# Optimization experiments

Measured on AMD Instinct MI355X. Metric: run time of the kernel, lower is better.

Reference implementation:

```python
import jax, jax.numpy as jnp
import numpy as np

N_NODES = 50000
N_EDGES = 800000
HID = 64
F_NODE = 64
F_EDGE = 16
DEC_H = 64
EPS = 1e-5


def setup_inputs() -> dict:
    key = jax.random.key(0)
    ks = jax.random.split(key, 16)
    inp = {}
    inp['x'] = jax.random.normal(ks[0], (N_NODES, F_NODE), dtype=jnp.float32)
    inp['edge_index'] = jax.random.randint(ks[1], (2, N_EDGES), 0, N_NODES, dtype=jnp.int32)
    inp['edge_attr'] = jax.random.normal(ks[2], (N_EDGES, F_EDGE), dtype=jnp.float32)
    # 3 GCN layers (F_NODE == HID so weights stack)
    inp['conv_w'] = jax.random.normal(ks[3], (3, HID, HID), dtype=jnp.float32) / np.sqrt(HID)
    inp['conv_b'] = jnp.zeros((3, HID), dtype=jnp.float32)
    inp['ln_g'] = jnp.ones((3, HID), dtype=jnp.float32)
    inp['ln_b'] = jnp.zeros((3, HID), dtype=jnp.float32)
    dec_in = 2 * HID + F_EDGE
    inp['dec_w1'] = jax.random.normal(ks[4], (dec_in, DEC_H), dtype=jnp.float32) / np.sqrt(dec_in)
    inp['dec_b1'] = jnp.zeros((DEC_H,), dtype=jnp.float32)
    inp['dec_w2'] = jax.random.normal(ks[5], (DEC_H, DEC_H // 2), dtype=jnp.float32) / np.sqrt(DEC_H)
    inp['dec_b2'] = jnp.zeros((DEC_H // 2,), dtype=jnp.float32)
    inp['dec_w3'] = jax.random.normal(ks[6], (DEC_H // 2, 1), dtype=jnp.float32) / np.sqrt(DEC_H // 2)
    inp['dec_b3'] = jnp.zeros((1,), dtype=jnp.float32)
    return inp


def _layer_norm(h, g, b):
    mu = jnp.mean(h, axis=-1, keepdims=True)
    var = jnp.mean(jnp.square(h - mu), axis=-1, keepdims=True)
    return (h - mu) * jax.lax.rsqrt(var + EPS) * g + b


def _forward(x, edge_index, edge_attr, conv_w, conv_b, ln_g, ln_b,
             dec_w1, dec_b1, dec_w2, dec_b2, dec_w3, dec_b3):
    n = x.shape[0]
    src, dst = edge_index[0], edge_index[1]
    # add self-loops (PyG GCNConv default)
    loop = jnp.arange(n, dtype=edge_index.dtype)
    src_sl = jnp.concatenate([src, loop])
    dst_sl = jnp.concatenate([dst, loop])
    # symmetric normalization: deg over target column (incl. self-loops)
    deg = jax.ops.segment_sum(jnp.ones_like(src_sl, dtype=x.dtype), dst_sl, num_segments=n)
    dinv = jnp.where(deg > 0, jax.lax.rsqrt(deg), 0.0)
    norm = dinv[src_sl] * dinv[dst_sl]  # (E+N,)

    h = x
    for l in range(conv_w.shape[0]):
        t = h @ conv_w[l]                                   # (N, H)
        msg = t[src_sl] * norm[:, None]                     # (E+N, H)
        agg = jax.ops.segment_sum(msg, dst_sl, num_segments=n) + conv_b[l]
        h = jax.nn.relu(_layer_norm(agg, ln_g[l], ln_b[l]))
        # dropout is identity at inference

    # edge decoder: concat(src_emb, dst_emb, edge_attr) -> MLP -> scalar
    z = jnp.concatenate([h[src], h[dst], edge_attr], axis=-1)  # (E, 2H+Fe)
    z = jax.nn.relu(z @ dec_w1 + dec_b1)
    z = jax.nn.relu(z @ dec_w2 + dec_b2)
    return (z @ dec_w3 + dec_b3).squeeze(-1)                   # (E,)


def reference(x, edge_index, edge_attr, conv_w, conv_b, ln_g, ln_b,
              dec_w1, dec_b1, dec_w2, dec_b2, dec_w3, dec_b3):
    return _forward(x, edge_index, edge_attr, conv_w, conv_b, ln_g, ln_b,
                    dec_w1, dec_b1, dec_w2, dec_b2, dec_w3, dec_b3)
```

## Files before the change

### kernel.cpp

```cpp
#include <hip/hip_runtime.h>
#include <hip/hip_fp16.h>

#define N_NODES 50000
#define N_EDGES 800000
#define HID 64
#define F_EDGE 16
#define LN_EPS 1e-5f
#define SCAN_BLOCKS ((N_NODES + 255) / 256)

__device__ inline float wave_sum64(float v) {
    #pragma unroll
    for (int o = 32; o > 0; o >>= 1) v += __shfl_xor(v, o, 64);
    return v;
}

__global__ void k_zero_cnt(int* __restrict__ cnt) {
    int i = blockIdx.x * blockDim.x + threadIdx.x;
    if (i < N_NODES) cnt[i] = 0;
}

__global__ void k_count(const int* __restrict__ dst, int* __restrict__ cnt) {
    int e = blockIdx.x * blockDim.x + threadIdx.x;
    if (e < N_EDGES) atomicAdd(&cnt[dst[e]], 1);
}

__global__ void k_scan1(const int* __restrict__ cnt, int* __restrict__ row_ptr,
                        int* __restrict__ bsum, float* __restrict__ dinv) {
    __shared__ int wsum[4];
    int tid = threadIdx.x, lane = tid & 63, w = tid >> 6;
    int i = blockIdx.x * 256 + tid;
    int v = (i < N_NODES) ? cnt[i] : 0;
    if (i < N_NODES) dinv[i] = rsqrtf((float)v + 1.0f);
    int isc = v;
    #pragma unroll
    for (int o = 1; o < 64; o <<= 1) {
        int n = __shfl_up(isc, o, 64);
        if (lane >= o) isc += n;
    }
    if (lane == 63) wsum[w] = isc;
    __syncthreads();
    int woff = 0;
    #pragma unroll
    for (int k = 0; k < 4; k++) woff += (k < w) ? wsum[k] : 0;
    if (i < N_NODES) row_ptr[i] = woff + isc - v;
    if (tid == 255) bsum[blockIdx.x] = woff + isc;
}

__global__ void k_scan2(const int* __restrict__ bsum, int* __restrict__ boff) {
    __shared__ int wsum[4];
    int tid = threadIdx.x, lane = tid & 63, w = tid >> 6;
    int v = (tid < SCAN_BLOCKS) ? bsum[tid] : 0;
    int isc = v;
    #pragma unroll
    for (int o = 1; o < 64; o <<= 1) {
        int n = __shfl_up(isc, o, 64);
        if (lane >= o) isc += n;
    }
    if (lane == 63) wsum[w] = isc;
    __syncthreads();
    int woff = 0;
    #pragma unroll
    for (int k = 0; k < 4; k++) woff += (k < w) ? wsum[k] : 0;
    if (tid < SCAN_BLOCKS) boff[tid] = woff + isc - v;
}

__global__ void k_scan3(int* __restrict__ row_ptr, const int* __restrict__ boff,
                        int* __restrict__ cursor) {
    int i = blockIdx.x * blockDim.x + threadIdx.x;
    if (i < N_NODES) {
        int r = row_ptr[i] + boff[i >> 8];
        row_ptr[i] = r;
        cursor[i] = r;
    }
    if (i == 0) row_ptr[N_NODES] = N_EDGES;
}

__global__ void k_fill(const int* __restrict__ src, const int* __restrict__ dst,
                       const float* __restrict__ dinv, int* __restrict__ cursor,
                       int* __restrict__ col, float* __restrict__ ew) {
    int e = blockIdx.x * blockDim.x + threadIdx.x;
    if (e < N_EDGES) {
        int s = src[e], d = dst[e];
        int pos = atomicAdd(&cursor[d], 1);
        col[pos] = s;
        ew[pos] = dinv[s] * dinv[d];
    }
}

__global__ void __launch_bounds__(256)
k_gemm_reg(const float* __restrict__ hin, const float* __restrict__ W,
           __half* __restrict__ out) {
    int lane = threadIdx.x & 63;
    int wid = (blockIdx.x * blockDim.x + threadIdx.x) >> 6;
    int nwaves = (gridDim.x * blockDim.x) >> 6;
    float w[64];
    #pragma unroll
    for (int k = 0; k < 64; k++) w[k] = W[k * 64 + lane];
    for (int row = wid; row < N_NODES; row += nwaves) {
        int r = __builtin_amdgcn_readfirstlane(row);
        const float* xr = hin + r * 64;
        float acc = 0.0f;
        #pragma unroll
        for (int k = 0; k < 64; k++) acc = fmaf(xr[k], w[k], acc);
        out[r * 64 + lane] = __float2half_rn(acc);
    }
}

__global__ void __launch_bounds__(256)
k_gemm_pq(const float* __restrict__ hin, const float* __restrict__ Wp,
          const float* __restrict__ bp, const float* __restrict__ Wq,
          __half* __restrict__ P, __half* __restrict__ Q) {
    int half_g = gridDim.x >> 1;
    bool isQ = (blockIdx.x >= half_g);
    const float* W = isQ ? Wq : Wp;
    __half* out = isQ ? Q : P;
    int lane = threadIdx.x & 63;
    int bid = isQ ? (blockIdx.x - half_g) : blockIdx.x;
    int wid = (bid * blockDim.x + threadIdx.x) >> 6;
    int nwaves = (half_g * blockDim.x) >> 6;
    float w[64];
    #pragma unroll
    for (int k = 0; k < 64; k++) w[k] = W[k * 64 + lane];
    float binit = isQ ? 0.0f : bp[lane];
    for (int row = wid; row < N_NODES; row += nwaves) {
        int r = __builtin_amdgcn_readfirstlane(row);
        const float* xr = hin + r * 64;
        float acc = binit;
        #pragma unroll
        for (int k = 0; k < 64; k++) acc = fmaf(xr[k], w[k], acc);
        out[r * 64 + lane] = __float2half_rn(acc);
    }
}

__global__ void __launch_bounds__(256)
k_gather_ln(const __half* __restrict__ t, const float* __restrict__ dinv,
            const int* __restrict__ row_ptr, const int* __restrict__ col,
            const float* __restrict__ ew, const float* __restrict__ cb,
            const float* __restrict__ g, const float* __restrict__ b,
            float* __restrict__ h) {
    int gid = blockIdx.x * blockDim.x + threadIdx.x;
    int node = gid >> 6, lane = gid & 63;
    if (node >= N_NODES) return;
    int n0 = __builtin_amdgcn_readfirstlane(node);
    int q = lane >> 3;
    int c8 = lane & 7;
    const float4* t4 = (const float4*)t;

    float acc[8];
    #pragma unroll
    for (int u = 0; u < 8; u++) acc[u] = 0.0f;

    if (q == 0) {
        float di = dinv[n0];
        float s2 = di * di;
        float4 raw = t4[(size_t)n0 * 8 + c8];
        const __half2* hp = (const __half2*)&raw;
        const float4* cb4 = (const float4*)cb;
        float4 cb0 = cb4[2 * c8], cb1 = cb4[2 * c8 + 1];
        float2 f0 = __half22float2(hp[0]);
        float2 f1 = __half22float2(hp[1]);
        float2 f2 = __half22float2(hp[2]);
        float2 f3 = __half22float2(hp[3]);
        acc[0] = fmaf(f0.x, s2, cb0.x); acc[1] = fmaf(f0.y, s2, cb0.y);
        acc[2] = fmaf(f1.x, s2, cb0.z); acc[3] = fmaf(f1.y, s2, cb0.w);
        acc[4] = fmaf(f2.x, s2, cb1.x); acc[5] = fmaf(f2.y, s2, cb1.y);
        acc[6] = fmaf(f3.x, s2, cb1.z); acc[7] = fmaf(f3.y, s2, cb1.w);
    }

    int beg = row_ptr[n0], end = row_ptr[n0 + 1];
    int deg = end - beg;

    int cL = 0; float wL = 0.0f;
    if (lane < deg) { cL = col[beg + lane]; wL = ew[beg + lane]; }
    int steps = (min(deg, 64) + 7) >> 3;

    #pragma unroll 4
    for (int st = 0; st < steps; st++) {
        int idx = 8 * st + q;
        int s = __shfl(cL, idx, 64);
        float wgt = __shfl(wL, idx, 64);
        float4 raw = t4[(size_t)s * 8 + c8];
        const __half2* hp = (const __half2*)&raw;
        float2 f0 = __half22float2(hp[0]);
        float2 f1 = __half22float2(hp[1]);
        float2 f2 = __half22float2(hp[2]);
        float2 f3 = __half22float2(hp[3]);
        acc[0] = fmaf(f0.x, wgt, acc[0]); acc[1] = fmaf(f0.y, wgt, acc[1]);
        acc[2] = fmaf(f1.x, wgt, acc[2]); acc[3] = fmaf(f1.y, wgt, acc[3]);
        acc[4] = fmaf(f2.x, wgt, acc[4]); acc[5] = fmaf(f2.y, wgt, acc[5]);
        acc[6] = fmaf(f3.x, wgt, acc[6]); acc[7] = fmaf(f3.y, wgt, acc[7]);
    }
    for (int j = beg + 64 + q; j < end; j += 8) {
        int s = col[j];
        float wgt = ew[j];
        float4 raw = t4[(size_t)s * 8 + c8];
        const __half2* hp = (const __half2*)&raw;
        float2 f0 = __half22float2(hp[0]);
        float2 f1 = __half22float2(hp[1]);
        float2 f2 = __half22float2(hp[2]);
        float2 f3 = __half22float2(hp[3]);
        acc[0] = fmaf(f0.x, wgt, acc[0]); acc[1] = fmaf(f0.y, wgt, acc[1]);
        acc[2] = fmaf(f1.x, wgt, acc[2]); acc[3] = fmaf(f1.y, wgt, acc[3]);
        acc[4] = fmaf(f2.x, wgt, acc[4]); acc[5] = fmaf(f2.y, wgt, acc[5]);
        acc[6] = fmaf(f3.x, wgt, acc[6]); acc[7] = fmaf(f3.y, wgt, acc[7]);
    }

    #pragma unroll
    for (int o = 8; o <= 32; o <<= 1) {
        #pragma unroll
        for (int u = 0; u < 8; u++) acc[u] += __shfl_xor(acc[u], o, 64);
    }

    float ps = 0.0f;
    #pragma unroll
    for (int u = 0; u < 8; u++) ps += acc[u];
    float mu = wave_sum64(ps) * (1.0f / 512.0f);
    float dd[8], vps = 0.0f;
    #pragma unroll
    for (int u = 0; u < 8; u++) { dd[u] = acc[u] - mu; vps += dd[u] * dd[u]; }
    float var = wave_sum64(vps) * (1.0f / 512.0f);
    float rstd = rsqrtf(var + LN_EPS);

    if (q == 0) {
        const float4* g4 = (const float4*)g;
        const float4* b4 = (const float4*)b;
        float4 g0 = g4[2 * c8], g1 = g4[2 * c8 + 1];
        float4 b0 = b4[2 * c8], b1v = b4[2 * c8 + 1];
        float4 y0, y1;
        y0.x = fmaxf(fmaf(dd[0] * rstd, g0.x, b0.x), 0.f);
        y0.y = fmaxf(fmaf(dd[1] * rstd, g0.y, b0.y), 0.f);
        y0.z = fmaxf(fmaf(dd[2] * rstd, g0.z, b0.z), 0.f);
        y0.w = fmaxf(fmaf(dd[3] * rstd, g0.w, b0.w), 0.f);
        y1.x = fmaxf(fmaf(dd[4] * rstd, g1.x, b1v.x), 0.f);
        y1.y = fmaxf(fmaf(dd[5] * rstd, g1.y, b1v.y), 0.f);
        y1.z = fmaxf(fmaf(dd[6] * rstd, g1.z, b1v.z), 0.f);
        y1.w = fmaxf(fmaf(dd[7] * rstd, g1.w, b1v.w), 0.f);
        float4* h4 = (float4*)h;
        h4[(size_t)n0 * 16 + 2 * c8] = y0;
        h4[(size_t)n0 * 16 + 2 * c8 + 1] = y1;
    }
}

__global__ void __launch_bounds__(256)
k_decoder(const __half* __restrict__ P, const __half* __restrict__ Q,
          const int* __restrict__ src, const int* __restrict__ dst,
          const float* __restrict__ attr,
          const float* __restrict__ W1c,
          const float* __restrict__ W2, const float* __restrict__ b2,
          const float* __restrict__ W3, const float* __restrict__ b3,
          float* __restrict__ out) {
    int e = blockIdx.x * blockDim.x + threadIdx.x;
    if (e >= N_EDGES) return;
    int s = src[e], d = dst[e];

    const float4* ap = (const float4*)(attr + (size_t)e * 16);
    float4 av0 = ap[0], av1 = ap[1], av2 = ap[2], av3 = ap[3];

    float acc[64];
    const float4* Pp = (const float4*)(P + (size_t)s * 64);
    const float4* Qp = (const float4*)(Q + (size_t)d * 64);
    #pragma unroll
    for (int c = 0; c < 8; c++) {
        float4 pv = Pp[c], qv = Qp[c];
        const __half2* ph = (const __half2*)&pv;
        const __half2* qh = (const __half2*)&qv;
        #pragma unroll
        for (int u = 0; u < 4; u++) {
            float2 pf = __half22float2(ph[u]);
            float2 qf = __half22float2(qh[u]);
            acc[8 * c + 2 * u]     = pf.x + qf.x;
            acc[8 * c + 2 * u + 1] = pf.y + qf.y;
        }
    }

    #pragma unroll
    for (int j = 0; j < 64; j++) {
        float a = acc[j];
        a = fmaf(av0.x, W1c[0 * 64 + j], a);
        a = fmaf(av0.y, W1c[1 * 64 + j], a);
        a = fmaf(av0.z, W1c[2 * 64 + j], a);
        a = fmaf(av0.w, W1c[3 * 64 + j], a);
        a = fmaf(av1.x, W1c[4 * 64 + j], a);
        a = fmaf(av1.y, W1c[5 * 64 + j], a);
        a = fmaf(av1.z, W1c[6 * 64 + j], a);
        a = fmaf(av1.w, W1c[7 * 64 + j], a);
        a = fmaf(av2.x, W1c[8 * 64 + j], a);
        a = fmaf(av2.y, W1c[9 * 64 + j], a);
        a = fmaf(av2.z, W1c[10 * 64 + j], a);
        a = fmaf(av2.w, W1c[11 * 64 + j], a);
        a = fmaf(av3.x, W1c[12 * 64 + j], a);
        a = fmaf(av3.y, W1c[13 * 64 + j], a);
        a = fmaf(av3.z, W1c[14 * 64 + j], a);
        a = fmaf(av3.w, W1c[15 * 64 + j], a);
        acc[j] = fmaxf(a, 0.0f);
    }

    float acc2[32];
    #pragma unroll
    for (int j = 0; j < 32; j++) acc2[j] = b2[j];
    #pragma unroll
    for (int k = 0; k < 64; k++) {
        float hk = acc[k];
        #pragma unroll
        for (int j = 0; j < 32; j++)
            acc2[j] = fmaf(hk, W2[k * 32 + j], acc2[j]);
    }

    float o = b3[0];
    #pragma unroll
    for (int j = 0; j < 32; j++)
        o = fmaf(fmaxf(acc2[j], 0.0f), W3[j], o);
    out[e] = o;
}

extern "C" void kernel_launch(void* const* d_in, const int* in_sizes, int n_in,
                              void* d_out, int out_size, void* d_ws, size_t ws_size,
                              hipStream_t stream) {
    const float* x      = (const float*)d_in[0];
    const int*   ei     = (const int*)d_in[1];
    const float* attr   = (const float*)d_in[2];
    const float* conv_w = (const float*)d_in[3];
    const float* conv_b = (const float*)d_in[4];
    const float* ln_g   = (const float*)d_in[5];
    const float* ln_b   = (const float*)d_in[6];
    const float* dw1    = (const float*)d_in[7];
    const float* db1    = (const float*)d_in[8];
    const float* dw2    = (const float*)d_in[9];
    const float* db2    = (const float*)d_in[10];
    const float* dw3    = (const float*)d_in[11];
    const float* db3    = (const float*)d_in[12];
    float* out = (float*)d_out;

    const int* src = ei;
    const int* dst = ei + N_EDGES;

    char* p = (char*)d_ws;
    float*  dinv    = (float*)p;  p += sizeof(float) * N_NODES;
    float*  h       = (float*)p;  p += sizeof(float) * (size_t)N_NODES * 64;
    __half* t_h     = (__half*)p; p += sizeof(__half) * (size_t)N_NODES * 64;
    __half* P_h     = (__half*)p; p += sizeof(__half) * (size_t)N_NODES * 64;
    __half* Q_h     = (__half*)p; p += sizeof(__half) * (size_t)N_NODES * 64;
    int*    cnt     = (int*)p;    p += sizeof(int) * N_NODES;
    int*    cursor  = (int*)p;    p += sizeof(int) * N_NODES;
    int*    row_ptr = (int*)p;    p += sizeof(int) * (N_NODES + 1);
    int*    col     = (int*)p;    p += sizeof(int) * N_EDGES;
    float*  ew      = (float*)p;  p += sizeof(float) * N_EDGES;
    int*    bsum    = (int*)p;    p += sizeof(int) * 256;
    int*    boff    = (int*)p;    p += sizeof(int) * 256;

    const int nb_nodes = (N_NODES + 255) / 256;
    const int nb_edges = (N_EDGES + 255) / 256;

    k_zero_cnt<<<nb_nodes, 256, 0, stream>>>(cnt);
    k_count<<<nb_edges, 256, 0, stream>>>(dst, cnt);
    k_scan1<<<SCAN_BLOCKS, 256, 0, stream>>>(cnt, row_ptr, bsum, dinv);
    k_scan2<<<1, 256, 0, stream>>>(bsum, boff);
    k_scan3<<<nb_nodes, 256, 0, stream>>>(row_ptr, boff, cursor);
    k_fill<<<nb_edges, 256, 0, stream>>>(src, dst, dinv, cursor, col, ew);

    const int gemm_blocks = 1024;
    const int gather_blocks = N_NODES / 4;

    const float* hin = x;
    for (int l = 0; l < 3; l++) {
        k_gemm_reg<<<gemm_blocks, 256, 0, stream>>>(hin, conv_w + l * 4096, t_h);
        k_gather_ln<<<gather_blocks, 256, 0, stream>>>(
            t_h, dinv, row_ptr, col, ew, conv_b + l * 64,
            ln_g + l * 64, ln_b + l * 64, h);
        hin = h;
    }

    k_gemm_pq<<<2 * gemm_blocks, 256, 0, stream>>>(h, dw1, db1, dw1 + 64 * 64, P_h, Q_h);

    k_decoder<<<nb_edges, 256, 0, stream>>>(
        P_h, Q_h, src, dst, attr, dw1 + 128 * 64, dw2, db2, dw3, db3, out);
}
```

Measured before the change: 476.9 us.

## Reorder GCN layer to aggregate pre-scaled features before GEMM and fuse LayerNorm

Each GCN layer now runs aggregate-then-transform. Node features are pre-scaled by dinv and stored as fp16, so the gather sums neighbours without per-edge weights, and the edge-weight array and its loads go away. LayerNorm, ReLU and bias move into the GEMM kernel, which writes the next layer's dinv-scaled fp16 features directly. The cost is an extra element-wise init kernel, an fp32 agg buffer written and read between the two kernels each layer, and fp16 storage of the pre-scaled inputs, which may change precision slightly.

```diff
diff --git a/kernel.cpp b/kernel.cpp
--- a/kernel.cpp
+++ b/kernel.cpp
@@ -76,33 +76,127 @@
 }
 
 __global__ void k_fill(const int* __restrict__ src, const int* __restrict__ dst,
-                       const float* __restrict__ dinv, int* __restrict__ cursor,
-                       int* __restrict__ col, float* __restrict__ ew) {
+                       int* __restrict__ cursor, int* __restrict__ col) {
     int e = blockIdx.x * blockDim.x + threadIdx.x;
     if (e < N_EDGES) {
         int s = src[e], d = dst[e];
         int pos = atomicAdd(&cursor[d], 1);
         col[pos] = s;
-        ew[pos] = dinv[s] * dinv[d];
-    }
+    }
+}
+
+__global__ void k_xs_init(const float* __restrict__ x, const float* __restrict__ dinv,
+                          __half* __restrict__ xs) {
+    int i = blockIdx.x * blockDim.x + threadIdx.x;
+    if (i < N_NODES * 64) xs[i] = __float2half_rn(x[i] * dinv[i >> 6]);
 }
 
 __global__ void __launch_bounds__(256)
-k_gemm_reg(const float* __restrict__ hin, const float* __restrict__ W,
-           __half* __restrict__ out) {
+k_gather_agg(const __half* __restrict__ xs, const float* __restrict__ dinv,
+             const int* __restrict__ row_ptr, const int* __restrict__ col,
+             float* __restrict__ agg) {
+    int gid = blockIdx.x * blockDim.x + threadIdx.x;
+    int node = gid >> 6, lane = gid & 63;
+    if (node >= N_NODES) return;
+    int n0 = __builtin_amdgcn_readfirstlane(node);
+    int q = lane >> 3;
+    int c8 = lane & 7;
+    const float4* x4 = (const float4*)xs;
+
+    float acc[8];
+    #pragma unroll
+    for (int u = 0; u < 8; u++) acc[u] = 0.0f;
+
+    if (q == 0) {
+        float4 raw = x4[(size_t)n0 * 8 + c8];
+        const __half2* hp = (const __half2*)&raw;
+        float2 f0 = __half22float2(hp[0]);
+        float2 f1 = __half22float2(hp[1]);
+        float2 f2 = __half22float2(hp[2]);
+        float2 f3 = __half22float2(hp[3]);
+        acc[0] = f0.x; acc[1] = f0.y; acc[2] = f1.x; acc[3] = f1.y;
+        acc[4] = f2.x; acc[5] = f2.y; acc[6] = f3.x; acc[7] = f3.y;
+    }
+
+    int beg = row_ptr[n0], end = row_ptr[n0 + 1];
+    int deg = end - beg;
+
+    int cL = 0;
+    if (lane < deg) cL = col[beg + lane];
+    int steps = (min(deg, 64) + 7) >> 3;
+
+    #pragma unroll 4
+    for (int st = 0; st < steps; st++) {
+        int idx = 8 * st + q;
+        int s = __shfl(cL, idx, 64);
+        float m = (idx < deg) ? 1.0f : 0.0f;
+        float4 raw = x4[(size_t)s * 8 + c8];
+        const __half2* hp = (const __half2*)&raw;
+        float2 f0 = __half22float2(hp[0]);
+        float2 f1 = __half22float2(hp[1]);
+        float2 f2 = __half22float2(hp[2]);
+        float2 f3 = __half22float2(hp[3]);
+        acc[0] = fmaf(f0.x, m, acc[0]); acc[1] = fmaf(f0.y, m, acc[1]);
+        acc[2] = fmaf(f1.x, m, acc[2]); acc[3] = fmaf(f1.y, m, acc[3]);
+        acc[4] = fmaf(f2.x, m, acc[4]); acc[5] = fmaf(f2.y, m, acc[5]);
+        acc[6] = fmaf(f3.x, m, acc[6]); acc[7] = fmaf(f3.y, m, acc[7]);
+    }
+    for (int j = beg + 64 + q; j < end; j += 8) {
+        int s = col[j];
+        float4 raw = x4[(size_t)s * 8 + c8];
+        const __half2* hp = (const __half2*)&raw;
+        float2 f0 = __half22float2(hp[0]);
+        float2 f1 = __half22float2(hp[1]);
+        float2 f2 = __half22float2(hp[2]);
+        float2 f3 = __half22float2(hp[3]);
+        acc[0] += f0.x; acc[1] += f0.y; acc[2] += f1.x; acc[3] += f1.y;
+        acc[4] += f2.x; acc[5] += f2.y; acc[6] += f3.x; acc[7] += f3.y;
+    }
+
+    #pragma unroll
+    for (int o = 8; o <= 32; o <<= 1) {
+        #pragma unroll
+        for (int u = 0; u < 8; u++) acc[u] += __shfl_xor(acc[u], o, 64);
+    }
+
+    if (q == 0) {
+        float di = dinv[n0];
+        float4 y0, y1;
+        y0.x = acc[0] * di; y0.y = acc[1] * di; y0.z = acc[2] * di; y0.w = acc[3] * di;
+        y1.x = acc[4] * di; y1.y = acc[5] * di; y1.z = acc[6] * di; y1.w = acc[7] * di;
+        float4* a4 = (float4*)agg;
+        a4[(size_t)n0 * 16 + 2 * c8] = y0;
+        a4[(size_t)n0 * 16 + 2 * c8 + 1] = y1;
+    }
+}
+
+__global__ void __launch_bounds__(256)
+k_gemm_ln(const float* __restrict__ agg, const float* __restrict__ W,
+          const float* __restrict__ cb, const float* __restrict__ g,
+          const float* __restrict__ b, const float* __restrict__ dinv,
+          __half* __restrict__ xs_out, float* __restrict__ h_out) {
     int lane = threadIdx.x & 63;
     int wid = (blockIdx.x * blockDim.x + threadIdx.x) >> 6;
     int nwaves = (gridDim.x * blockDim.x) >> 6;
     float w[64];
     #pragma unroll
     for (int k = 0; k < 64; k++) w[k] = W[k * 64 + lane];
+    float cbl = cb[lane], gl = g[lane], bl = b[lane];
     for (int row = wid; row < N_NODES; row += nwaves) {
         int r = __builtin_amdgcn_readfirstlane(row);
-        const float* xr = hin + r * 64;
-        float acc = 0.0f;
+        const float* xr = agg + r * 64;
+        float acc = cbl;
         #pragma unroll
         for (int k = 0; k < 64; k++) acc = fmaf(xr[k], w[k], acc);
-        out[r * 64 + lane] = __float2half_rn(acc);
+        float mu = wave_sum64(acc) * (1.0f / 64.0f);
+        float d = acc - mu;
+        float var = wave_sum64(d * d) * (1.0f / 64.0f);
+        float y = fmaxf(fmaf(d * rsqrtf(var + LN_EPS), gl, bl), 0.0f);
+        if (xs_out) {
+            xs_out[r * 64 + lane] = __float2half_rn(y * dinv[r]);
+        } else {
+            h_out[r * 64 + lane] = y;
+        }
     }
 }
 
@@ -129,115 +223,6 @@
         #pragma unroll
         for (int k = 0; k < 64; k++) acc = fmaf(xr[k], w[k], acc);
         out[r * 64 + lane] = __float2half_rn(acc);
-    }
-}
-
-__global__ void __launch_bounds__(256)
-k_gather_ln(const __half* __restrict__ t, const float* __restrict__ dinv,
-            const int* __restrict__ row_ptr, const int* __restrict__ col,
-            const float* __restrict__ ew, const float* __restrict__ cb,
-            const float* __restrict__ g, const float* __restrict__ b,
-            float* __restrict__ h) {
-    int gid = blockIdx.x * blockDim.x + threadIdx.x;
-    int node = gid >> 6, lane = gid & 63;
-    if (node >= N_NODES) return;
-    int n0 = __builtin_amdgcn_readfirstlane(node);
-    int q = lane >> 3;
-    int c8 = lane & 7;
-    const float4* t4 = (const float4*)t;
-
-    float acc[8];
-    #pragma unroll
-    for (int u = 0; u < 8; u++) acc[u] = 0.0f;
-
-    if (q == 0) {
-        float di = dinv[n0];
-        float s2 = di * di;
-        float4 raw = t4[(size_t)n0 * 8 + c8];
-        const __half2* hp = (const __half2*)&raw;
-        const float4* cb4 = (const float4*)cb;
-        float4 cb0 = cb4[2 * c8], cb1 = cb4[2 * c8 + 1];
-        float2 f0 = __half22float2(hp[0]);
-        float2 f1 = __half22float2(hp[1]);
-        float2 f2 = __half22float2(hp[2]);
-        float2 f3 = __half22float2(hp[3]);
-        acc[0] = fmaf(f0.x, s2, cb0.x); acc[1] = fmaf(f0.y, s2, cb0.y);
-        acc[2] = fmaf(f1.x, s2, cb0.z); acc[3] = fmaf(f1.y, s2, cb0.w);
-        acc[4] = fmaf(f2.x, s2, cb1.x); acc[5] = fmaf(f2.y, s2, cb1.y);
-        acc[6] = fmaf(f3.x, s2, cb1.z); acc[7] = fmaf(f3.y, s2, cb1.w);
-    }
-
-    int beg = row_ptr[n0], end = row_ptr[n0 + 1];
-    int deg = end - beg;
-
-    int cL = 0; float wL = 0.0f;
-    if (lane < deg) { cL = col[beg + lane]; wL = ew[beg + lane]; }
-    int steps = (min(deg, 64) + 7) >> 3;
-
-    #pragma unroll 4
-    for (int st = 0; st < steps; st++) {
-        int idx = 8 * st + q;
-        int s = __shfl(cL, idx, 64);
-        float wgt = __shfl(wL, idx, 64);
-        float4 raw = t4[(size_t)s * 8 + c8];
-        const __half2* hp = (const __half2*)&raw;
-        float2 f0 = __half22float2(hp[0]);
-        float2 f1 = __half22float2(hp[1]);
-        float2 f2 = __half22float2(hp[2]);
-        float2 f3 = __half22float2(hp[3]);
-        acc[0] = fmaf(f0.x, wgt, acc[0]); acc[1] = fmaf(f0.y, wgt, acc[1]);
-        acc[2] = fmaf(f1.x, wgt, acc[2]); acc[3] = fmaf(f1.y, wgt, acc[3]);
-        acc[4] = fmaf(f2.x, wgt, acc[4]); acc[5] = fmaf(f2.y, wgt, acc[5]);
-        acc[6] = fmaf(f3.x, wgt, acc[6]); acc[7] = fmaf(f3.y, wgt, acc[7]);
-    }
-    for (int j = beg + 64 + q; j < end; j += 8) {
-        int s = col[j];
-        float wgt = ew[j];
-        float4 raw = t4[(size_t)s * 8 + c8];
-        const __half2* hp = (const __half2*)&raw;
-        float2 f0 = __half22float2(hp[0]);
-        float2 f1 = __half22float2(hp[1]);
-        float2 f2 = __half22float2(hp[2]);
-        float2 f3 = __half22float2(hp[3]);
-        acc[0] = fmaf(f0.x, wgt, acc[0]); acc[1] = fmaf(f0.y, wgt, acc[1]);
-        acc[2] = fmaf(f1.x, wgt, acc[2]); acc[3] = fmaf(f1.y, wgt, acc[3]);
-        acc[4] = fmaf(f2.x, wgt, acc[4]); acc[5] = fmaf(f2.y, wgt, acc[5]);
-        acc[6] = fmaf(f3.x, wgt, acc[6]); acc[7] = fmaf(f3.y, wgt, acc[7]);
-    }
-
-    #pragma unroll
-    for (int o = 8; o <= 32; o <<= 1) {
-        #pragma unroll
-        for (int u = 0; u < 8; u++) acc[u] += __shfl_xor(acc[u], o, 64);
-    }
-
-    float ps = 0.0f;
-    #pragma unroll
-    for (int u = 0; u < 8; u++) ps += acc[u];
-    float mu = wave_sum64(ps) * (1.0f / 512.0f);
-    float dd[8], vps = 0.0f;
-    #pragma unroll
-    for (int u = 0; u < 8; u++) { dd[u] = acc[u] - mu; vps += dd[u] * dd[u]; }
-    float var = wave_sum64(vps) * (1.0f / 512.0f);
-    float rstd = rsqrtf(var + LN_EPS);
-
-    if (q == 0) {
-        const float4* g4 = (const float4*)g;
-        const float4* b4 = (const float4*)b;
-        float4 g0 = g4[2 * c8], g1 = g4[2 * c8 + 1];
-        float4 b0 = b4[2 * c8], b1v = b4[2 * c8 + 1];
-        float4 y0, y1;
-        y0.x = fmaxf(fmaf(dd[0] * rstd, g0.x, b0.x), 0.f);
-        y0.y = fmaxf(fmaf(dd[1] * rstd, g0.y, b0.y), 0.f);
-        y0.z = fmaxf(fmaf(dd[2] * rstd, g0.z, b0.z), 0.f);
-        y0.w = fmaxf(fmaf(dd[3] * rstd, g0.w, b0.w), 0.f);
-        y1.x = fmaxf(fmaf(dd[4] * rstd, g1.x, b1v.x), 0.f);
-        y1.y = fmaxf(fmaf(dd[5] * rstd, g1.y, b1v.y), 0.f);
-        y1.z = fmaxf(fmaf(dd[6] * rstd, g1.z, b1v.z), 0.f);
-        y1.w = fmaxf(fmaf(dd[7] * rstd, g1.w, b1v.w), 0.f);
-        float4* h4 = (float4*)h;
-        h4[(size_t)n0 * 16 + 2 * c8] = y0;
-        h4[(size_t)n0 * 16 + 2 * c8 + 1] = y1;
     }
 }
 
@@ -336,41 +321,43 @@
 
     char* p = (char*)d_ws;
     float*  dinv    = (float*)p;  p += sizeof(float) * N_NODES;
-    float*  h       = (float*)p;  p += sizeof(float) * (size_t)N_NODES * 64;
-    __half* t_h     = (__half*)p; p += sizeof(__half) * (size_t)N_NODES * 64;
+    float*  agg     = (float*)p;  p += sizeof(float) * (size_t)N_NODES * 64;
+    float*  h3      = (float*)p;  p += sizeof(float) * (size_t)N_NODES * 64;
+    __half* xs      = (__half*)p; p += sizeof(__half) * (size_t)N_NODES * 64;
     __half* P_h     = (__half*)p; p += sizeof(__half) * (size_t)N_NODES * 64;
     __half* Q_h     = (__half*)p; p += sizeof(__half) * (size_t)N_NODES * 64;
     int*    cnt     = (int*)p;    p += sizeof(int) * N_NODES;
     int*    cursor  = (int*)p;    p += sizeof(int) * N_NODES;
     int*    row_ptr = (int*)p;    p += sizeof(int) * (N_NODES + 1);
     int*    col     = (int*)p;    p += sizeof(int) * N_EDGES;
-    float*  ew      = (float*)p;  p += sizeof(float) * N_EDGES;
     int*    bsum    = (int*)p;    p += sizeof(int) * 256;
     int*    boff    = (int*)p;    p += sizeof(int) * 256;
 
     const int nb_nodes = (N_NODES + 255) / 256;
     const int nb_edges = (N_EDGES + 255) / 256;
+    const int nb_elems = (N_NODES * 64 + 255) / 256;
 
     k_zero_cnt<<<nb_nodes, 256, 0, stream>>>(cnt);
     k_count<<<nb_edges, 256, 0, stream>>>(dst, cnt);
     k_scan1<<<SCAN_BLOCKS, 256, 0, stream>>>(cnt, row_ptr, bsum, dinv);
     k_scan2<<<1, 256, 0, stream>>>(bsum, boff);
     k_scan3<<<nb_nodes, 256, 0, stream>>>(row_ptr, boff, cursor);
-    k_fill<<<nb_edges, 256, 0, stream>>>(src, dst, dinv, cursor, col, ew);
+    k_fill<<<nb_edges, 256, 0, stream>>>(src, dst, cursor, col);
+    k_xs_init<<<nb_elems, 256, 0, stream>>>(x, dinv, xs);
 
     const int gemm_blocks = 1024;
     const int gather_blocks = N_NODES / 4;
 
-    const float* hin = x;
     for (int l = 0; l < 3; l++) {
-        k_gemm_reg<<<gemm_blocks, 256, 0, stream>>>(hin, conv_w + l * 4096, t_h);
-        k_gather_ln<<<gather_blocks, 256, 0, stream>>>(
-            t_h, dinv, row_ptr, col, ew, conv_b + l * 64,
-            ln_g + l * 64, ln_b + l * 64, h);
-        hin = h;
-    }
-
-    k_gemm_pq<<<2 * gemm_blocks, 256, 0, stream>>>(h, dw1, db1, dw1 + 64 * 64, P_h, Q_h);
+        k_gather_agg<<<gather_blocks, 256, 0, stream>>>(xs, dinv, row_ptr, col, agg);
+        bool last = (l == 2);
+        k_gemm_ln<<<gemm_blocks, 256, 0, stream>>>(
+            agg, conv_w + l * 4096, conv_b + l * 64,
+            ln_g + l * 64, ln_b + l * 64, dinv,
+            last ? (__half*)nullptr : xs, last ? h3 : (float*)nullptr);
+    }
+
+    k_gemm_pq<<<2 * gemm_blocks, 256, 0, stream>>>(h3, dw1, db1, dw1 + 64 * 64, P_h, Q_h);
 
     k_decoder<<<nb_edges, 256, 0, stream>>>(
         P_h, Q_h, src, dst, attr, dw1 + 128 * 64, dw2, db2, dw3, db3, out);
```

After: 465.7 us. -2.3%, faster.
